# Optimization experiments

Hardware: AMD Instinct MI355X
Metric: run time of the kernel (lower is better)

The kernel has to match this reference:

```python
import jax, jax.numpy as jnp
import numpy as np

K = 98          # fixed_n_tokens
HEADS = 8
EPS = 1e-5      # BatchNorm eps


def setup_inputs() -> dict:
    key = jax.random.key(0)
    ks = jax.random.split(key, 8)
    B, C, H, W = 32, 384, 56, 56

    def p(k, shape, scale=0.02):
        return jax.random.normal(k, shape, jnp.float32) * scale

    return {
        "x": jax.random.normal(ks[0], (B, C, H, W), jnp.float32),
        "qkv_w": p(ks[1], (3 * C, C)),
        "qkv_b": jnp.zeros((3 * C,), jnp.float32),
        "proj_w": p(ks[2], (C, C)),
        "proj_b": jnp.zeros((C,), jnp.float32),
        "bn_g": jnp.ones((C,), jnp.float32),
        "bn_b": jnp.zeros((C,), jnp.float32),
        "fc1_w": p(ks[3], (C, C)),
        "fc1_b": jnp.zeros((C,), jnp.float32),
        "fc2_w": p(ks[4], (C, C)),
        "fc2_b": jnp.zeros((C,), jnp.float32),
        "dw_w": p(ks[5], (C, 1, 3, 3), 0.1),  # depthwise 3x3, groups=C
        "dw_b": jnp.zeros((C,), jnp.float32),
    }


def reference(x, qkv_w, qkv_b, proj_w, proj_b, bn_g, bn_b,
              fc1_w, fc1_b, fc2_w, fc2_b, dw_w, dw_b):
    B, C, H, W = x.shape
    N = H * W
    head_dim = C // HEADS
    scale = head_dim ** -0.5

    # ---- salience top-k selection (pool_size=(1,1): no pooling) ----
    xf = x.reshape(B, C, N)
    scores = jnp.sum(xf * xf, axis=1)                       # [B, N]
    _, top_idx = jax.lax.top_k(scores, K)                   # [B, K]
    top = jnp.take_along_axis(xf, top_idx[:, None, :], axis=2)   # [B, C, K]
    bg = (xf.sum(2) - top.sum(2)) / (N - K)                 # [B, C]
    tokens = jnp.concatenate([top, bg[:, :, None]], axis=2)      # [B, C, K+1]
    tokens = tokens.transpose(0, 2, 1)                      # [B, K+1, C]

    # ---- tiny attention over K+1 tokens ----
    n = K + 1
    qkv = tokens @ qkv_w.T + qkv_b                          # [B, n, 3C]
    qkv = qkv.reshape(B, n, 3, HEADS, head_dim).transpose(2, 0, 3, 1, 4)
    q, k, v = qkv[0], qkv[1], qkv[2]                        # [B, h, n, d]
    attn = jax.nn.softmax(scale * jnp.einsum('bhnd,bhmd->bhnm', q, k), axis=-1)
    res = jnp.einsum('bhnm,bhmd->bhnd', attn, v)            # [B, h, n, d]
    attn_out = res.transpose(0, 1, 3, 2).reshape(B, C, n)   # b (h d) n

    # ---- scatter-restore: bg token everywhere, top tokens at their slots ----
    top_res, bg_res = attn_out[:, :, :K], attn_out[:, :, K:]    # [B,C,K], [B,C,1]
    restored = jnp.broadcast_to(bg_res, (B, C, N))
    bi = jnp.arange(B)[:, None, None]
    ci = jnp.arange(C)[None, :, None]
    restored = restored.at[bi, ci, top_idx[:, None, :]].set(top_res)
    restored = restored.reshape(B, C, H, W)  # interpolate is identity (same size)

    # ---- conv branch: BN (batch stats) -> fc1 -> gelu -> dwconv -> fc2 ----
    mu = x.mean(axis=(0, 2, 3), keepdims=True)
    var = x.var(axis=(0, 2, 3), keepdims=True)
    xn = (x - mu) * jax.lax.rsqrt(var + EPS)
    xn = xn * bn_g[None, :, None, None] + bn_b[None, :, None, None]
    h1 = jnp.einsum('bchw,oc->bohw', xn, fc1_w) + fc1_b[None, :, None, None]
    h1 = jax.nn.gelu(h1, approximate=False)
    h2 = jax.lax.conv_general_dilated(
        h1, dw_w, window_strides=(1, 1), padding='SAME',
        dimension_numbers=('NCHW', 'OIHW', 'NCHW'), feature_group_count=C)
    h2 = h2 + dw_b[None, :, None, None]
    conv_out = jnp.einsum('bchw,oc->bohw', h2, fc2_w) + fc2_b[None, :, None, None]

    combined = restored + conv_out
    return jnp.einsum('bchw,oc->bohw', combined, proj_w) + proj_b[None, :, None, None]
```

## Files before the change

### kernel.cpp

```cpp
#include <hip/hip_runtime.h>
#include <hip/hip_bf16.h>
#include <math.h>

typedef unsigned short u16;
typedef short short8 __attribute__((ext_vector_type(8)));
typedef float floatx4 __attribute__((ext_vector_type(4)));

#define B_    32
#define C_    384
#define N_    3136
#define K_TOP 98
#define NTOK  99
#define TOKS  (B_ * NTOK)
#define HEADS_ 8
#define HD    48
#define KDIM  384

__device__ __forceinline__ float b2f(u16 u) {
    unsigned int x = ((unsigned int)u) << 16;
    return __builtin_bit_cast(float, x);
}
__device__ __forceinline__ u16 f2b(float f) {
    unsigned int x = __builtin_bit_cast(unsigned int, f);
    unsigned int r = (x + 0x7fffu + ((x >> 16) & 1u)) >> 16;
    return (u16)r;
}
__device__ __forceinline__ u16 tob16(float f) { return f2b(f); }
__device__ __forceinline__ u16 tob16(u16 u) { return u; }


__global__ void k_zero(float* sumsq) { sumsq[threadIdx.x] = 0.f; }

__global__ void k_cvt(const float* __restrict__ src, u16* __restrict__ dst, int n) {
    int i = blockIdx.x * 256 + threadIdx.x;
    if (i < n) dst[i] = f2b(src[i]);
}

__global__ void k_scores(const float* __restrict__ x, float* __restrict__ scores) {
    int gid = blockIdx.x * 256 + threadIdx.x;
    int b = gid / N_;
    int p = gid - b * N_;
    const float* xp = x + (size_t)b * C_ * N_ + p;
    float s = 0.f;
#pragma unroll 8
    for (int c = 0; c < C_; ++c) {
        float v = xp[(size_t)c * N_];
        s += v * v;
    }
    scores[gid] = s;
}

__global__ void k_chsum(const float* __restrict__ x, float* __restrict__ ch_sum,
                        float* __restrict__ sumsq) {
    int bc = blockIdx.x;
    int c = bc % C_;
    const float* xp = x + (size_t)bc * N_;
    float s1 = 0.f, s2 = 0.f;
    for (int p = threadIdx.x; p < N_; p += 256) {
        float v = xp[p];
        s1 += v; s2 += v * v;
    }
#pragma unroll
    for (int off = 32; off; off >>= 1) {
        s1 += __shfl_down(s1, off);
        s2 += __shfl_down(s2, off);
    }
    __shared__ float r1[4], r2[4];
    int wave = threadIdx.x >> 6;
    if ((threadIdx.x & 63) == 0) { r1[wave] = s1; r2[wave] = s2; }
    __syncthreads();
    if (threadIdx.x == 0) {
        float a = r1[0] + r1[1] + r1[2] + r1[3];
        float b2 = r2[0] + r2[1] + r2[2] + r2[3];
        ch_sum[bc] = a;
        atomicAdd(&sumsq[c], b2);
    }
}

__launch_bounds__(1024)
__global__ void k_topk(const float* __restrict__ scores, int* __restrict__ idx,
                       int* __restrict__ istop) {
    int b = blockIdx.x;
    int tid = threadIdx.x;
    __shared__ unsigned int keys[N_];
    __shared__ int hist[4096];
    __shared__ unsigned int sh_prefix;
    __shared__ int sh_g;
    __shared__ int c1, tc;
    __shared__ int idxbuf[K_TOP];
    __shared__ int tiebuf[128];

    for (int p = tid; p < N_; p += 1024) {
        keys[p] = __builtin_bit_cast(unsigned int, scores[b * N_ + p]);
        istop[b * N_ + p] = 0;
    }

    int Kcur = K_TOP;
    unsigned int prefix = 0;
    int m = 0;
#pragma unroll
    for (int pass = 0; pass < 3; ++pass) {
        const int shift = (pass == 0) ? 20 : (pass == 1 ? 8 : 0);
        const int nbins = (pass == 2) ? 256 : 4096;
        const unsigned int pm = (pass == 0) ? 0u : (pass == 1 ? 0xFFF00000u : 0xFFFFFF00u);
        for (int i = tid; i < nbins; i += 1024) hist[i] = 0;
        __syncthreads();
        for (int p = tid; p < N_; p += 1024) {
            unsigned int u = keys[p];
            if ((u & pm) == prefix) atomicAdd(&hist[(u >> shift) & (nbins - 1)], 1);
        }
        __syncthreads();
        if (tid < 64) {
            int lane = tid;
            int nch = nbins >> 6;
            int s = 0;
            for (int j = 0; j < nch; ++j) s += hist[lane * nch + j];
            int suf = s;
#pragma unroll
            for (int off = 1; off < 64; off <<= 1) {
                int v = __shfl_down(suf, off);
                if (lane + off < 64) suf += v;
            }
            int above = suf - s;
            if (suf >= Kcur && above < Kcur) {
                int acc = above;
                int bin = (lane + 1) * nch - 1;
                for (;; --bin) {
                    int h = hist[bin];
                    if (acc + h >= Kcur) break;
                    acc += h;
                }
                sh_prefix = prefix | ((unsigned int)bin << shift);
                sh_g = acc;
            }
        }
        __syncthreads();
        prefix = sh_prefix;
        m += sh_g;
        Kcur -= sh_g;
    }

    unsigned int lo = prefix;
    if (tid == 0) { c1 = 0; tc = 0; }
    __syncthreads();
    for (int p = tid; p < N_; p += 1024) {
        unsigned int u = keys[p];
        if (u > lo) { int pos = atomicAdd(&c1, 1); idxbuf[pos] = p; }
        else if (u == lo) { int pos = atomicAdd(&tc, 1); if (pos < 128) tiebuf[pos] = p; }
    }
    __syncthreads();
    if (tid == 0) {
        int need = K_TOP - m;
        if (tc <= 128) {
            int cnt = tc;
            for (int r = 0; r < need; ++r) {
                int mi = r;
                for (int q = r + 1; q < cnt; ++q) if (tiebuf[q] < tiebuf[mi]) mi = q;
                int t = tiebuf[mi]; tiebuf[mi] = tiebuf[r]; tiebuf[r] = t;
                idxbuf[m + r] = t;
            }
        } else {
            int picked = 0;
            for (int p = 0; p < N_ && picked < need; ++p)
                if (keys[p] == lo) { idxbuf[m + picked] = p; ++picked; }
        }
    }
    __syncthreads();
    if (tid < K_TOP) {
        int ib = idxbuf[tid];
        idx[b * K_TOP + tid] = ib;
        istop[b * N_ + ib] = tid + 1;
    }
}

__launch_bounds__(256)
__global__ void k_tokens(const float* __restrict__ x, const int* __restrict__ idx,
                         const float* __restrict__ ch_sum, u16* __restrict__ tokensT) {
    int b = blockIdx.x, cg = blockIdx.y;
    __shared__ int il[K_TOP];
    int tid = threadIdx.x;
    if (tid < K_TOP) il[tid] = idx[b * K_TOP + tid];
    __syncthreads();
    int cl = tid >> 2;
    int js = tid & 3;
    int c = cg * 64 + cl;
    const float* xp = x + (size_t)b * C_ * N_ + (size_t)c * N_;
    u16* tp = tokensT + (size_t)c * TOKS + b * NTOK;
    float s = 0.f;
    for (int j = js; j < K_TOP; j += 4) {
        float v = xp[il[j]];
        tp[j] = f2b(v);
        s += v;
    }
    s += __shfl_down(s, 2);
    s += __shfl_down(s, 1);
    if (js == 0) {
        float bg = (ch_sum[b * C_ + c] - s) * (1.0f / (float)(N_ - K_TOP));
        tp[K_TOP] = f2b(bg);
    }
}

__global__ void k_bnfin(const float* ch_sum, const float* sumsq, const float* bn_g,
                        const float* bn_b, float* a_scale, float* b_shift) {
    int c = threadIdx.x;
    float s = 0.f;
    for (int b = 0; b < B_; ++b) s += ch_sum[b * C_ + c];
    float inv_n = 1.0f / (float)(B_ * N_);
    float mu = s * inv_n;
    float var = sumsq[c] * inv_n - mu * mu;
    float a = rsqrtf(var + 1e-5f) * bn_g[c];
    a_scale[c] = a;
    b_shift[c] = bn_b[c] - mu * a;
}

__global__ void k_bias2p(const float* __restrict__ fc2_w, const float* __restrict__ fc2_b,
                         const float* __restrict__ dw_b, float* __restrict__ bias2p) {
    int c = blockIdx.x * 4 + (threadIdx.x >> 6);
    int l = threadIdx.x & 63;
    float acc = 0.f;
    for (int k = l; k < C_; k += 64) acc += fc2_w[c * C_ + k] * dw_b[k];
#pragma unroll
    for (int off = 32; off; off >>= 1) acc += __shfl_down(acc, off);
    if (l == 0) bias2p[c] = acc + fc2_b[c];
}

__global__ void k_biasM(const float* __restrict__ proj_w, const float* __restrict__ proj_b,
                        const float* __restrict__ bias2p, float* __restrict__ biasM) {
    int o = blockIdx.x * 4 + (threadIdx.x >> 6);
    int l = threadIdx.x & 63;
    float acc = 0.f;
    for (int c = l; c < C_; c += 64) acc += proj_w[o * C_ + c] * bias2p[c];
#pragma unroll
    for (int off = 32; off; off >>= 1) acc += __shfl_down(acc, off);
    if (l == 0) biasM[o] = acc + proj_b[o];
}

__global__ void k_bias1(const float* __restrict__ fc1_w, const float* __restrict__ fc1_b,
                        const float* __restrict__ b_shift, float* __restrict__ bias1) {
    int o = blockIdx.x * 4 + (threadIdx.x >> 6);
    int l = threadIdx.x & 63;
    float acc = 0.f;
    for (int c = l; c < C_; c += 64) acc += fc1_w[o * C_ + c] * b_shift[c];
#pragma unroll
    for (int off = 32; off; off >>= 1) acc += __shfl_down(acc, off);
    if (l == 0) bias1[o] = acc + fc1_b[o];
}

__global__ void k_cbias(const float* __restrict__ proj_w, const float* __restrict__ biasM,
                        const float* __restrict__ bgres, float* __restrict__ cbias) {
    int b = blockIdx.y;
    int o = blockIdx.x * 4 + (threadIdx.x >> 6);
    int l = threadIdx.x & 63;
    float acc = 0.f;
    for (int c = l; c < C_; c += 64) acc += proj_w[o * C_ + c] * bgres[b * C_ + c];
#pragma unroll
    for (int off = 32; off; off >>= 1) acc += __shfl_down(acc, off);
    if (l == 0) cbias[b * C_ + o] = acc + biasM[o];
}

__global__ void k_mw(const float* __restrict__ proj_w, const float* __restrict__ fc2_w,
                     u16* __restrict__ Mw) {
    int o = blockIdx.x, c = threadIdx.x;
    float acc = 0.f;
    for (int k = 0; k < C_; ++k) acc += proj_w[o * C_ + k] * fc2_w[k * C_ + c];
    Mw[o * C_ + c] = f2b(acc);
}

__global__ void k_w1p(const float* fc1_w, const float* a_scale, u16* W1p) {
    int i = blockIdx.x * 256 + threadIdx.x;
    if (i < C_ * C_) {
        int c = i % C_;
        W1p[i] = f2b(fc1_w[i] * a_scale[c]);
    }
}

__launch_bounds__(256)
__global__ void k_gemm_qkv(const u16* __restrict__ A, const u16* __restrict__ Bsrc,
                           const float* __restrict__ biasB, float* __restrict__ outF) {
    const int ldB = TOKS, NC = TOKS;
    int m0 = blockIdx.x * 128;
    int n0 = blockIdx.y * 64;
    int tid = threadIdx.x;
    int lane = tid & 63;
    int wave = tid >> 6;
    int wm0 = (wave >> 1) * 64;
    int wn0 = (wave & 1) * 32;
    int lm = lane & 15;
    int quad = lane >> 4;

    __shared__ __attribute__((aligned(16))) u16 Al[128 * 32];
    __shared__ __attribute__((aligned(16))) u16 Bl[64 * 32];

    floatx4 acc[4][2];
#pragma unroll
    for (int i = 0; i < 4; ++i)
#pragma unroll
        for (int j = 0; j < 2; ++j)
#pragma unroll
            for (int r = 0; r < 4; ++r) acc[i][j][r] = 0.f;

    int ar = tid >> 2;
    int akc = (tid & 3) * 8;
    int bp = tid & 63;
    int bgi = tid >> 6;
    int bswz = ((bgi ^ ((bp >> 1) & 3)) & 3) * 8;
    int bcol = n0 + bp;
    bool bok = bcol < NC;

    for (int kt = 0; kt < 12; ++kt) {
        int k0 = kt * 32;
        __syncthreads();
#pragma unroll
        for (int i = 0; i < 2; ++i) {
            int r = ar + i * 64;
            short8 v = *(const short8*)(const void*)(A + (size_t)(m0 + r) * KDIM + k0 + akc);
            *(short8*)(void*)&Al[r * 32 + akc] = v;
        }
        {
            const u16* src = Bsrc + (size_t)(k0 + bgi * 8) * ldB + bcol;
            short8 v;
#pragma unroll
            for (int j = 0; j < 8; ++j)
                v[j] = bok ? (short)src[(size_t)j * ldB] : (short)0;
            *(short8*)(void*)&Bl[bp * 32 + bswz] = v;
        }
        __syncthreads();
        short8 af[4], bfv[2];
#pragma unroll
        for (int mt = 0; mt < 4; ++mt)
            af[mt] = *(const short8*)(const void*)&Al[(wm0 + mt * 16 + lm) * 32 + quad * 8];
#pragma unroll
        for (int nt = 0; nt < 2; ++nt) {
            int prow = wn0 + nt * 16 + lm;
            int sw = ((quad ^ ((prow >> 1) & 3)) & 3) * 8;
            bfv[nt] = *(const short8*)(const void*)&Bl[prow * 32 + sw];
        }
#pragma unroll
        for (int mt = 0; mt < 4; ++mt)
#pragma unroll
            for (int nt = 0; nt < 2; ++nt)
                acc[mt][nt] = __builtin_amdgcn_mfma_f32_16x16x32_bf16(af[mt], bfv[nt], acc[mt][nt], 0, 0, 0);
    }

#pragma unroll
    for (int nt = 0; nt < 2; ++nt) {
        int col = n0 + wn0 + nt * 16 + lm;
        if (col >= NC) continue;
#pragma unroll
        for (int mt = 0; mt < 4; ++mt)
#pragma unroll
            for (int r = 0; r < 4; ++r) {
                int o = m0 + wm0 + mt * 16 + quad * 4 + r;
                outF[(size_t)o * TOKS + col] = acc[mt][nt][r] + biasB[o];
            }
    }
}

template<int MODE, typename TB>
__launch_bounds__(512, 2)
__global__ void k_gemm2(const u16* __restrict__ A, const TB* __restrict__ B0, long bStride,
                        const float* __restrict__ biasF,
                        float* __restrict__ outF,
                        u16* __restrict__ outB,
                        const float* __restrict__ cbias, const int* __restrict__ istop,
                        const float* __restrict__ delta2) {
    const int ldB = N_;
    int b = blockIdx.y;
    int n0 = blockIdx.x * 64;
    const TB* Bsrc = B0 + (size_t)b * bStride;
    int tid = threadIdx.x;
    int lane = tid & 63;
    int wave = tid >> 6;
    int wm0 = wave * 48;
    int lm = lane & 15;
    int quad = lane >> 4;

    __shared__ __attribute__((aligned(16))) u16 Bl[64 * 384];

    {
        int sc = tid & 63;
        int kg = tid >> 6;
        const TB* bp = Bsrc + (size_t)n0 + sc;
        TB rv[48];
#pragma unroll
        for (int m = 0; m < 6; ++m)
#pragma unroll
            for (int j = 0; j < 8; ++j)
                rv[m * 8 + j] = bp[(size_t)(kg * 48 + m * 8 + j) * ldB];
#pragma unroll
        for (int m = 0; m < 6; ++m) {
            int win = kg * 6 + m;
            short8 s;
#pragma unroll
            for (int j = 0; j < 8; ++j) s[j] = (short)tob16(rv[m * 8 + j]);
            *(short8*)(void*)&Bl[sc * 384 + ((win ^ (sc & 7)) * 8)] = s;
        }
    }

    floatx4 acc[3][4];
#pragma unroll
    for (int i = 0; i < 3; ++i)
#pragma unroll
        for (int j = 0; j < 4; ++j)
#pragma unroll
            for (int r = 0; r < 4; ++r) acc[i][j][r] = 0.f;

    __syncthreads();

    const u16* Ap = A + (size_t)(wm0 + lm) * KDIM + quad * 8;
    short8 af[3], afn[3];
#pragma unroll
    for (int mt = 0; mt < 3; ++mt)
        af[mt] = *(const short8*)(const void*)(Ap + (size_t)(mt * 16) * KDIM);

    for (int kt = 0; kt < 12; ++kt) {
        if (kt < 11) {
#pragma unroll
            for (int mt = 0; mt < 3; ++mt)
                afn[mt] = *(const short8*)(const void*)(Ap + (size_t)(mt * 16) * KDIM + (kt + 1) * 32);
        }
        short8 bfv[4];
#pragma unroll
        for (int nt = 0; nt < 4; ++nt) {
            int pc = nt * 16 + lm;
            int win = kt * 4 + quad;
            bfv[nt] = *(const short8*)(const void*)&Bl[pc * 384 + ((win ^ (pc & 7)) * 8)];
        }
#pragma unroll
        for (int mt = 0; mt < 3; ++mt)
#pragma unroll
            for (int nt = 0; nt < 4; ++nt)
                acc[mt][nt] = __builtin_amdgcn_mfma_f32_16x16x32_bf16(af[mt], bfv[nt], acc[mt][nt], 0, 0, 0);
#pragma unroll
        for (int mt = 0; mt < 3; ++mt) af[mt] = afn[mt];
    }

    if (MODE == 1) {
        __syncthreads();
        u16* hls = Bl;
#pragma unroll
        for (int nt = 0; nt < 4; ++nt)
#pragma unroll
            for (int mt = 0; mt < 3; ++mt)
#pragma unroll
                for (int r = 0; r < 4; ++r) {
                    int o = wm0 + mt * 16 + quad * 4 + r;
                    float val = acc[mt][nt][r] + biasF[o];
                    float g = 0.5f * val * (1.0f + erff(val * 0.70710678118654752f));
                    hls[o * 64 + nt * 16 + lm] = f2b(g);
                }
        __syncthreads();
        int row0 = tid >> 3;
        int cg = (tid & 7) * 8;
        u16* dst = outB + (size_t)b * C_ * N_ + n0;
#pragma unroll
        for (int it = 0; it < 6; ++it) {
            int row = it * 64 + row0;
            short8 v = *(const short8*)(const void*)&hls[row * 64 + cg];
            *(short8*)(void*)(dst + (size_t)row * N_ + cg) = v;
        }
    } else {
#pragma unroll
        for (int nt = 0; nt < 4; ++nt) {
            int ocol = n0 + nt * 16 + lm;
            int tt = 0;
            if (MODE == 3) tt = istop[b * N_ + ocol];
#pragma unroll
            for (int mt = 0; mt < 3; ++mt) {
#pragma unroll
                for (int r = 0; r < 4; ++r) {
                    int o = wm0 + mt * 16 + quad * 4 + r;
                    float val = acc[mt][nt][r];
                    if (MODE == 2) {
                        outF[(size_t)o * N_ + ocol] = val;
                    } else {
                        val += cbias[b * C_ + o];
                        if (tt) val += delta2[(size_t)o * N_ + b * K_TOP + (tt - 1)];
                        outF[(size_t)b * C_ * N_ + (size_t)o * N_ + ocol] = val;
                    }
                }
            }
        }
    }
}


__global__ void k_attn_scores(const float* __restrict__ qkv, float* __restrict__ Sws) {
    int b = blockIdx.x, h = blockIdx.y;
    __shared__ float ql[NTOK * HD], kl[NTOK * HD];
    int tid = threadIdx.x;
    const float scale = 0.14433756729740643f;
    for (int u = tid; u < NTOK * HD; u += 256) {
        int d = u / NTOK, j = u - d * NTOK;
        size_t base = (size_t)(h * HD + d) * TOKS + b * NTOK + j;
        ql[j * HD + d] = qkv[base] * scale;
        kl[j * HD + d] = qkv[base + (size_t)C_ * TOKS];
    }
    __syncthreads();
    float* Sp = Sws + (size_t)(b * HEADS_ + h) * (NTOK * NTOK);
    for (int u = tid; u < NTOK * NTOK; u += 256) {
        int i = u / NTOK, j = u - i * NTOK;
        float s = 0.f;
#pragma unroll 8
        for (int d = 0; d < HD; ++d) s += ql[i * HD + d] * kl[j * HD + d];
        Sp[u] = s;
    }
}

__global__ void k_attn_out(const float* __restrict__ qkv, const float* __restrict__ Sws,
                           u16* __restrict__ diffT, float* __restrict__ bgres) {
    int b = blockIdx.x, h = blockIdx.y;
    __shared__ float vl[NTOK * HD];
    __shared__ float P[NTOK * 100];
    __shared__ float bgrow[HD];
    int tid = threadIdx.x;
    for (int u = tid; u < NTOK * HD; u += 256) {
        int d = u / NTOK, j = u - d * NTOK;
        vl[j * HD + d] = qkv[(size_t)(2 * C_ + h * HD + d) * TOKS + b * NTOK + j];
    }
    __syncthreads();
    const float* Sp = Sws + (size_t)(b * HEADS_ + h) * (NTOK * NTOK);
    if (tid < NTOK) {
        int i = tid;
        float mx = -1e30f;
        for (int j = 0; j < NTOK; ++j) mx = fmaxf(mx, Sp[i * NTOK + j]);
        float sum = 0.f;
        for (int j = 0; j < NTOK; ++j) { float e = expf(Sp[i * NTOK + j] - mx); P[i * 100 + j] = e; sum += e; }
        float inv = 1.f / sum;
        for (int j = 0; j < NTOK; ++j) P[i * 100 + j] *= inv;
    }
    __syncthreads();
    if (tid < HD) {
        int d = tid;
        float a = 0.f;
        for (int j = 0; j < NTOK; ++j) a += P[K_TOP * 100 + j] * vl[j * HD + d];
        bgrow[d] = a;
        bgres[b * C_ + h * HD + d] = a;
    }
    __syncthreads();
    for (int u = tid; u < K_TOP * HD; u += 256) {
        int d = u / K_TOP, i = u - d * K_TOP;
        float a = 0.f;
        for (int j = 0; j < NTOK; ++j) a += P[i * 100 + j] * vl[j * HD + d];
        diffT[(size_t)(h * HD + d) * N_ + b * K_TOP + i] = f2b(a - bgrow[d]);
    }
}

__launch_bounds__(256)
__global__ void k_dwconv(u16* __restrict__ h1, const float* __restrict__ dw_w) {
    int bc = blockIdx.x;
    int c = bc % C_;
    __shared__ __attribute__((aligned(16))) u16 tile[4256];
    int tid = threadIdx.x;
#pragma unroll
    for (int i = tid; i < 532; i += 256)
        *(short8*)(void*)&tile[i * 8] = (short8)0;
    float w[9];
#pragma unroll
    for (int t = 0; t < 9; ++t) w[t] = dw_w[c * 9 + t];
    __syncthreads();
    u16* src = h1 + (size_t)bc * N_;
    for (int i = tid; i < 392; i += 256) {
        int y = i / 7, xg = i - y * 7;
        short8 v = *(const short8*)(const void*)(src + i * 8);
        *(short8*)(void*)&tile[(y + 2) * 72 + xg * 8] = v;
    }
    __syncthreads();
    for (int g = tid; g < 392; g += 256) {
        int y = g / 7, xg = (g - y * 7) * 8;
        float out[8];
#pragma unroll
        for (int t = 0; t < 8; ++t) out[t] = 0.f;
#pragma unroll
        for (int ky = 0; ky < 3; ++ky) {
            const u16* rp = &tile[(y + ky + 1) * 72 + xg];
            short8 mid = *(const short8*)(const void*)rp;
            float r[10];
            r[0] = b2f(rp[-1]);
#pragma unroll
            for (int t = 0; t < 8; ++t) r[t + 1] = b2f((u16)mid[t]);
            r[9] = b2f(rp[8]);
#pragma unroll
            for (int kx = 0; kx < 3; ++kx) {
                float wv = w[ky * 3 + kx];
#pragma unroll
                for (int t = 0; t < 8; ++t) out[t] += wv * r[t + kx];
            }
        }
        short8 o;
#pragma unroll
        for (int t = 0; t < 8; ++t) o[t] = (short)f2b(out[t]);
        *(short8*)(void*)(src + g * 8) = o;
    }
}


extern "C" void kernel_launch(void* const* d_in, const int* in_sizes, int n_in,
                              void* d_out, int out_size, void* d_ws, size_t ws_size,
                              hipStream_t stream) {
    (void)in_sizes; (void)n_in; (void)out_size; (void)ws_size;
    const float* x      = (const float*)d_in[0];
    const float* qkv_w  = (const float*)d_in[1];
    const float* qkv_b  = (const float*)d_in[2];
    const float* proj_w = (const float*)d_in[3];
    const float* proj_b = (const float*)d_in[4];
    const float* bn_g   = (const float*)d_in[5];
    const float* bn_b   = (const float*)d_in[6];
    const float* fc1_w  = (const float*)d_in[7];
    const float* fc1_b  = (const float*)d_in[8];
    const float* fc2_w  = (const float*)d_in[9];
    const float* fc2_b  = (const float*)d_in[10];
    const float* dw_w   = (const float*)d_in[11];
    const float* dw_b   = (const float*)d_in[12];
    float* out = (float*)d_out;

    float* qkvF = (float*)d_out;
    float* Sws  = (float*)((char*)d_out + (size_t)3 * C_ * TOKS * 4);

    char* w = (char*)d_ws;
    constexpr size_t o_h1      = 0;
    constexpr size_t o_scores  = o_h1      + (size_t)B_ * C_ * N_ * 2;
    constexpr size_t o_chsum   = o_scores  + (size_t)B_ * N_ * 4;
    constexpr size_t o_sumsq   = o_chsum   + (size_t)B_ * C_ * 4;
    constexpr size_t o_idx     = o_sumsq   + (size_t)C_ * 4;
    constexpr size_t o_istop   = o_idx     + (size_t)B_ * K_TOP * 4;
    constexpr size_t o_tokens  = o_istop   + (size_t)B_ * N_ * 4;
    constexpr size_t o_ascale  = o_tokens  + (size_t)C_ * TOKS * 2;
    constexpr size_t o_bshift  = o_ascale  + (size_t)C_ * 4;
    constexpr size_t o_w1p     = o_bshift  + (size_t)C_ * 4;
    constexpr size_t o_bias1   = o_w1p     + (size_t)C_ * C_ * 2;
    constexpr size_t o_mw      = o_bias1   + (size_t)C_ * 4;
    constexpr size_t o_biasM   = o_mw      + (size_t)C_ * C_ * 2;
    constexpr size_t o_bias2p  = o_biasM   + (size_t)C_ * 4;
    constexpr size_t o_cbias   = o_bias2p  + (size_t)C_ * 4;
    constexpr size_t o_bgres   = o_cbias   + (size_t)B_ * C_ * 4;
    constexpr size_t o_difft   = o_bgres   + (size_t)B_ * C_ * 4;
    constexpr size_t o_delta2  = o_difft   + (size_t)C_ * N_ * 2;
    constexpr size_t o_wq16    = o_delta2  + (size_t)C_ * N_ * 4;
    constexpr size_t o_pw16    = o_wq16    + (size_t)3 * C_ * C_ * 2;

    u16*   h1      = (u16*)(w + o_h1);
    float* scores  = (float*)(w + o_scores);
    float* ch_sum  = (float*)(w + o_chsum);
    float* sumsq   = (float*)(w + o_sumsq);
    int*   idx     = (int*)(w + o_idx);
    int*   istop   = (int*)(w + o_istop);
    u16*   tokensT = (u16*)(w + o_tokens);
    float* a_scale = (float*)(w + o_ascale);
    float* b_shift = (float*)(w + o_bshift);
    u16*   W1p     = (u16*)(w + o_w1p);
    float* bias1   = (float*)(w + o_bias1);
    u16*   Mw      = (u16*)(w + o_mw);
    float* biasM   = (float*)(w + o_biasM);
    float* bias2p  = (float*)(w + o_bias2p);
    float* cbias   = (float*)(w + o_cbias);
    float* bgres   = (float*)(w + o_bgres);
    u16*   diffT   = (u16*)(w + o_difft);
    float* Delta2  = (float*)(w + o_delta2);
    u16*   Wq16    = (u16*)(w + o_wq16);
    u16*   Pw16    = (u16*)(w + o_pw16);

    k_zero<<<1, C_, 0, stream>>>(sumsq);
    k_scores<<<(B_ * N_) / 256, 256, 0, stream>>>(x, scores);
    k_chsum<<<B_ * C_, 256, 0, stream>>>(x, ch_sum, sumsq);
    k_topk<<<B_, 1024, 0, stream>>>(scores, idx, istop);
    k_tokens<<<dim3(B_, 6), 256, 0, stream>>>(x, idx, ch_sum, tokensT);
    k_bnfin<<<1, C_, 0, stream>>>(ch_sum, sumsq, bn_g, bn_b, a_scale, b_shift);
    k_bias2p<<<96, 256, 0, stream>>>(fc2_w, fc2_b, dw_b, bias2p);
    k_mw<<<C_, C_, 0, stream>>>(proj_w, fc2_w, Mw);
    k_biasM<<<96, 256, 0, stream>>>(proj_w, proj_b, bias2p, biasM);
    k_w1p<<<(C_ * C_ + 255) / 256, 256, 0, stream>>>(fc1_w, a_scale, W1p);
    k_bias1<<<96, 256, 0, stream>>>(fc1_w, fc1_b, b_shift, bias1);
    k_cvt<<<(3 * C_ * C_ + 255) / 256, 256, 0, stream>>>(qkv_w, Wq16, 3 * C_ * C_);
    k_cvt<<<(C_ * C_ + 255) / 256, 256, 0, stream>>>(proj_w, Pw16, C_ * C_);

    k_gemm_qkv<<<dim3(9, 50), 256, 0, stream>>>(Wq16, tokensT, qkv_b, qkvF);
    k_attn_scores<<<dim3(B_, HEADS_), 256, 0, stream>>>(qkvF, Sws);
    k_attn_out<<<dim3(B_, HEADS_), 256, 0, stream>>>(qkvF, Sws, diffT, bgres);
    k_cbias<<<dim3(96, B_), 256, 0, stream>>>(proj_w, biasM, bgres, cbias);
    k_gemm2<2, u16><<<dim3(49, 1), 512, 0, stream>>>(Pw16, diffT, 0,
        nullptr, Delta2, nullptr, nullptr, nullptr, nullptr);
    k_gemm2<1, float><<<dim3(49, 32), 512, 0, stream>>>(W1p, x, (long)C_ * N_,
        bias1, nullptr, h1, nullptr, nullptr, nullptr);
    k_dwconv<<<B_ * C_, 256, 0, stream>>>(h1, dw_w);
    k_gemm2<3, u16><<<dim3(49, 32), 512, 0, stream>>>(Mw, h1, (long)C_ * N_,
        nullptr, out, nullptr, cbias, istop, Delta2);
}
```

Baseline: 721.4 us.

## Load GEMM B fragments directly from global memory instead of staging in LDS

Removes the shared-memory staging of the 64x384 B tile in k_gemm2. Each wave now loads its own B fragments from global memory with strided scalar loads, converts them to bf16, and double-buffers them across k-steps. LDS is kept only for the MODE 1 GELU epilogue, and launch bounds are raised to target 4 blocks per CU. This gives up cross-wave reuse of B, since all 8 waves in a block now re-read the same B columns, and uses uncoalesced column-strided loads that may raise global/L2 traffic and register pressure.

```diff
diff --git a/kernel.cpp b/kernel.cpp
--- a/kernel.cpp
+++ b/kernel.cpp
@@ -357,7 +357,7 @@
 }
 
 template<int MODE, typename TB>
-__launch_bounds__(512, 2)
+__launch_bounds__(512, 4)
 __global__ void k_gemm2(const u16* __restrict__ A, const TB* __restrict__ B0, long bStride,
                         const float* __restrict__ biasF,
                         float* __restrict__ outF,
@@ -375,27 +375,7 @@
     int lm = lane & 15;
     int quad = lane >> 4;
 
-    __shared__ __attribute__((aligned(16))) u16 Bl[64 * 384];
-
-    {
-        int sc = tid & 63;
-        int kg = tid >> 6;
-        const TB* bp = Bsrc + (size_t)n0 + sc;
-        TB rv[48];
-#pragma unroll
-        for (int m = 0; m < 6; ++m)
-#pragma unroll
-            for (int j = 0; j < 8; ++j)
-                rv[m * 8 + j] = bp[(size_t)(kg * 48 + m * 8 + j) * ldB];
-#pragma unroll
-        for (int m = 0; m < 6; ++m) {
-            int win = kg * 6 + m;
-            short8 s;
-#pragma unroll
-            for (int j = 0; j < 8; ++j) s[j] = (short)tob16(rv[m * 8 + j]);
-            *(short8*)(void*)&Bl[sc * 384 + ((win ^ (sc & 7)) * 8)] = s;
-        }
-    }
+    __shared__ __attribute__((aligned(16))) u16 hls[(MODE == 1) ? (C_ * 64) : 8];
 
     floatx4 acc[3][4];
 #pragma unroll
@@ -405,10 +385,19 @@
 #pragma unroll
             for (int r = 0; r < 4; ++r) acc[i][j][r] = 0.f;
 
-    __syncthreads();
-
     const u16* Ap = A + (size_t)(wm0 + lm) * KDIM + quad * 8;
-    short8 af[3], afn[3];
+    const TB* Bp = Bsrc + (size_t)(quad * 8) * ldB + n0 + lm;
+
+    short8 af[3], afn[3], bf[4], bfn[4];
+
+#pragma unroll
+    for (int nt = 0; nt < 4; ++nt) {
+        const TB* p = Bp + nt * 16;
+        short8 v;
+#pragma unroll
+        for (int j = 0; j < 8; ++j) v[j] = (short)tob16(p[(size_t)j * ldB]);
+        bf[nt] = v;
+    }
 #pragma unroll
     for (int mt = 0; mt < 3; ++mt)
         af[mt] = *(const short8*)(const void*)(Ap + (size_t)(mt * 16) * KDIM);
@@ -416,28 +405,29 @@
     for (int kt = 0; kt < 12; ++kt) {
         if (kt < 11) {
 #pragma unroll
+            for (int nt = 0; nt < 4; ++nt) {
+                const TB* p = Bp + (size_t)((kt + 1) * 32) * ldB + nt * 16;
+                short8 v;
+#pragma unroll
+                for (int j = 0; j < 8; ++j) v[j] = (short)tob16(p[(size_t)j * ldB]);
+                bfn[nt] = v;
+            }
+#pragma unroll
             for (int mt = 0; mt < 3; ++mt)
                 afn[mt] = *(const short8*)(const void*)(Ap + (size_t)(mt * 16) * KDIM + (kt + 1) * 32);
         }
-        short8 bfv[4];
-#pragma unroll
-        for (int nt = 0; nt < 4; ++nt) {
-            int pc = nt * 16 + lm;
-            int win = kt * 4 + quad;
-            bfv[nt] = *(const short8*)(const void*)&Bl[pc * 384 + ((win ^ (pc & 7)) * 8)];
-        }
 #pragma unroll
         for (int mt = 0; mt < 3; ++mt)
 #pragma unroll
             for (int nt = 0; nt < 4; ++nt)
-                acc[mt][nt] = __builtin_amdgcn_mfma_f32_16x16x32_bf16(af[mt], bfv[nt], acc[mt][nt], 0, 0, 0);
+                acc[mt][nt] = __builtin_amdgcn_mfma_f32_16x16x32_bf16(af[mt], bf[nt], acc[mt][nt], 0, 0, 0);
 #pragma unroll
         for (int mt = 0; mt < 3; ++mt) af[mt] = afn[mt];
+#pragma unroll
+        for (int nt = 0; nt < 4; ++nt) bf[nt] = bfn[nt];
     }
 
     if (MODE == 1) {
-        __syncthreads();
-        u16* hls = Bl;
 #pragma unroll
         for (int nt = 0; nt < 4; ++nt)
 #pragma unroll
```

After: 769.4 us. 1.07x slower.
